# Kernel optimization log

Measured on AMD Instinct MI355X. Metric: run time of the kernel, lower is better.

Reference implementation:

```python
import jax, jax.numpy as jnp
import numpy as np
from jax import lax

EPS = 1e-5

def setup_inputs() -> dict:
    key = jax.random.key(0)
    k1, k2 = jax.random.split(key)
    x = jax.random.normal(k1, (8, 256, 64, 64), dtype=jnp.float32)
    W = jax.random.normal(k2, (128, 256, 5, 5), dtype=jnp.float32) * 0.02
    gamma = jnp.ones((128,), dtype=jnp.float32)
    beta = jnp.zeros((128,), dtype=jnp.float32)
    return {"x": x, "W": W, "gamma": gamma, "beta": beta}

def reference(x, W, gamma, beta):
    B, C, H, Wd = x.shape
    # bilinear x2 upsample, half-pixel centers (== torch align_corners=False)
    up = jax.image.resize(x, (B, C, 2 * H, 2 * Wd), method="bilinear")
    # conv2d, stride 1, padding 2, no bias (norm == 'BN')
    out = lax.conv_general_dilated(
        up, W, window_strides=(1, 1), padding=[(2, 2), (2, 2)],
        dimension_numbers=("NCHW", "OIHW", "NCHW"))
    # BatchNorm2d (batch statistics, training-style refresh)
    mean = jnp.mean(out, axis=(0, 2, 3))
    var = jnp.var(out, axis=(0, 2, 3))
    inv = gamma / jnp.sqrt(var + EPS)
    out = (out - mean[None, :, None, None]) * inv[None, :, None, None] + beta[None, :, None, None]
    # activation: torch.relu
    return jax.nn.relu(out)
```

## Files before the change

kernel.cpp:

```cpp
#include <hip/hip_runtime.h>
#include <hip/hip_bf16.h>
#include <stdint.h>

typedef short s8v __attribute__((ext_vector_type(8)));
typedef float f4v __attribute__((ext_vector_type(4)));

__device__ __align__(16) float g_zeros[4] = {0.f, 0.f, 0.f, 0.f};

__device__ __forceinline__ void async_copy16(const void* gsrc, void* lds_dst) {
  __builtin_amdgcn_global_load_lds(
      (const __attribute__((address_space(1))) uint32_t*)(uintptr_t)gsrc,
      (__attribute__((address_space(3))) uint32_t*)(uint32_t)(uintptr_t)lds_dst,
      16, 0, 0);
}

__global__ void wpack_kernel(const float* __restrict__ W, __hip_bfloat16* __restrict__ Wr) {
  int i = blockIdx.x * 256 + threadIdx.x;
  int ci = i & 255;
  int rest = i >> 8;
  int co = rest & 127;
  int pos = rest >> 7;
  Wr[i] = __float2bfloat16(W[(co * 256 + ci) * 25 + pos]);
}

__global__ __launch_bounds__(256, 2) void upsample_kernel(const float* __restrict__ x,
                                                          __hip_bfloat16* __restrict__ up) {
  __shared__ __hip_bfloat16 lx[10 * 48 * 66];
  const int tid = threadIdx.x;
  const int bx = blockIdx.x;
  const int owb = bx & 1;
  const int ohb = (bx >> 1) & 7;
  const int cb = (bx >> 4) & 3;
  const int b = bx >> 6;
  const int oh0 = ohb * 16, ow0 = owb * 64, c0 = cb * 64;
  const int ih0 = (oh0 >> 1) - 1;
  const int iw_lo = (ow0 >> 1) - 1;
  const int aligned = (iw_lo < 0 ? 0 : iw_lo) & ~15;

  for (int i = tid; i < 64 * 10 * 12; i += 256) {
    int c = i / 120;
    int rem = i - c * 120;
    int r = rem / 12;
    int w4 = (rem - r * 12) * 4;
    int gr = ih0 + r;
    gr = gr < 0 ? 0 : (gr > 63 ? 63 : gr);
    const float4 v = *(const float4*)&x[(((b * 256 + c0 + c) * 64) + gr) * 64 + aligned + w4];
    int base = (r * 48 + w4) * 66 + c;
    lx[base]       = __float2bfloat16(v.x);
    lx[base + 66]  = __float2bfloat16(v.y);
    lx[base + 132] = __float2bfloat16(v.z);
    lx[base + 198] = __float2bfloat16(v.w);
  }
  __syncthreads();

  const int c2 = (tid & 31) * 2;
  const int owq = tid >> 5;
  uint32_t* upu = (uint32_t*)up;
  for (int it = 0; it < 128; ++it) {
    int oh_l = it >> 3;
    int ow_l = (it & 7) * 8 + owq;
    int oh = oh0 + oh_l, ow = ow0 + ow_l;
    int ihA = (oh >> 1) - ((oh & 1) ^ 1);
    float wh = (oh & 1) ? 0.75f : 0.25f;
    int iwA = (ow >> 1) - ((ow & 1) ^ 1);
    float wwt = (ow & 1) ? 0.75f : 0.25f;
    int r0 = ihA - ih0;
    int w0 = (iwA < 0 ? 0 : iwA) - aligned;
    int w1t = iwA + 1; w1t = w1t > 63 ? 63 : w1t;
    int w1 = w1t - aligned;
    uint32_t t00 = *(const uint32_t*)&lx[(r0 * 48 + w0) * 66 + c2];
    uint32_t t01 = *(const uint32_t*)&lx[(r0 * 48 + w1) * 66 + c2];
    uint32_t t10 = *(const uint32_t*)&lx[((r0 + 1) * 48 + w0) * 66 + c2];
    uint32_t t11 = *(const uint32_t*)&lx[((r0 + 1) * 48 + w1) * 66 + c2];
    float wlo = wh * wwt, wlo1 = wh * (1.f - wwt);
    float whi = (1.f - wh) * wwt, whi1 = (1.f - wh) * (1.f - wwt);
    float vlo = wlo * __uint_as_float(t00 << 16) + wlo1 * __uint_as_float(t01 << 16) +
                whi * __uint_as_float(t10 << 16) + whi1 * __uint_as_float(t11 << 16);
    float vhi = wlo * __uint_as_float(t00 & 0xffff0000u) + wlo1 * __uint_as_float(t01 & 0xffff0000u) +
                whi * __uint_as_float(t10 & 0xffff0000u) + whi1 * __uint_as_float(t11 & 0xffff0000u);
    __hip_bfloat16 h0 = __float2bfloat16(vlo);
    __hip_bfloat16 h1 = __float2bfloat16(vhi);
    uint32_t pk = (uint32_t)(*(unsigned short*)&h0) | ((uint32_t)(*(unsigned short*)&h1) << 16);
    upu[((((size_t)(b * 128 + oh) * 128) + ow) * 256 + c0 + c2) >> 1] = pk;
  }
}

#define ASLOT 4608
__global__ __launch_bounds__(512, 4) void conv_kernel(const __hip_bfloat16* __restrict__ up,
                                                      const __hip_bfloat16* __restrict__ Wr,
                                                      float* __restrict__ out,
                                                      float* __restrict__ gstats) {
  __shared__ __align__(16) unsigned short lA[5 * ASLOT];
  __shared__ __align__(16) unsigned short lB[2][128 * 64];
  __shared__ float lsum[128], lssq[128];

  const int tid = threadIdx.x;
  const int lane = tid & 63;
  const int wave = tid >> 6;
  const int wm = wave >> 1;
  const int wn = wave & 1;
  const int lane15 = lane & 15;
  const int quad = lane >> 4;

  const int bid = blockIdx.x;
  const int orig = ((bid & 7) << 6) | (bid >> 3);
  const int b = orig >> 6;
  const int oh0 = ((orig >> 1) & 31) << 2;
  const int owh = orig & 1;
  const int ow0 = owh << 6;

  const f4v zero4 = {0.f, 0.f, 0.f, 0.f};
  if (tid < 128) { lsum[tid] = 0.f; lssq[tid] = 0.f; }
  if (owh == 0) {
    for (int i = tid; i < 5 * 32; i += 512) {
      int s = i >> 5, rem = i & 31;
      *(f4v*)&lA[(s * 576 + (rem >> 3) * 8 + (rem & 7)) * 8] = zero4;
    }
  } else {
    for (int i = tid; i < 5 * 48; i += 512) {
      int s = i / 48, rem = i - s * 48;
      *(f4v*)&lA[(s * 576 + (66 + (rem >> 3)) * 8 + (rem & 7)) * 8] = zero4;
    }
  }

  auto stageA = [&](int slot, const __hip_bfloat16* uprow) {
    int idx = (wave << 6) + lane;
    int r = idx >> 3, pc = idx & 7;
    int cq = pc ^ (r & 7);
    int iw = ow0 - 4 + r;
    const void* src = ((unsigned)iw < 128u) ? (const void*)(uprow + iw * 256 + cq * 8)
                                            : (const void*)g_zeros;
    async_copy16(src, (void*)&lA[(slot * 576 + (wave << 6)) * 8]);
    if (wave == 0) {
      int idx2 = 512 + lane;
      int r2 = idx2 >> 3, pc2 = idx2 & 7;
      int cq2 = pc2 ^ (r2 & 7);
      int iw2 = ow0 - 4 + r2;
      const void* src2 = ((unsigned)iw2 < 128u) ? (const void*)(uprow + iw2 * 256 + cq2 * 8)
                                                : (const void*)g_zeros;
      async_copy16(src2, (void*)&lA[(slot * 576 + 512) * 8]);
    }
  };
  auto stageB = [&](const __hip_bfloat16* wrow, int bsel) {
#pragma unroll
    for (int t = 0; t < 2; ++t) {
      int base = t * 512 + (wave << 6);
      int idx = base + lane;
      int n = idx >> 3, pc = idx & 7;
      int cq = pc ^ (n & 7);
      async_copy16(wrow + n * 256 + cq * 8, (void*)&lB[bsel][base * 8]);
    }
  };

  f4v acc[4][4];
#pragma unroll
  for (int i = 0; i < 4; ++i)
#pragma unroll
    for (int j = 0; j < 4; ++j) acc[i][j] = zero4;

  for (int rr = 0; rr < 4; ++rr) {
    int ih = oh0 + rr - 2;
    if ((unsigned)ih < 128u)
      stageA(ih % 5, up + (size_t)(b * 128 + ih) * 128 * 256);
  }
  stageB(Wr, 0);
  __syncthreads();

  int buf = 0;
  for (int cb = 0; cb < 4; ++cb) {
    const int c0 = cb << 6;
    for (int kh = 0; kh < 5; ++kh) {
      const int ih = oh0 + wm + kh - 2;
      const bool rowok = (unsigned)ih < 128u;
      const int abase = rowok ? (ih % 5) * ASLOT : 0;
      for (int kw = 0; kw < 5; ++kw) {
        const int pos = kh * 5 + kw;
        if (pos < 24) {
          stageB(Wr + (size_t)(pos + 1) * 32768 + c0, buf ^ 1);
        } else if (cb < 3) {
          stageB(Wr + (c0 + 64), buf ^ 1);
        }
        if (kw == 2 && kh < 4) {
          int ihp = oh0 + kh + 2;
          if (ihp < 128)
            stageA(ihp % 5, up + (size_t)(b * 128 + ihp) * 128 * 256 + c0);
        }
        if (rowok) {
#pragma unroll
          for (int ks = 0; ks < 2; ++ks) {
            const int cq = ks * 4 + quad;
            s8v a[4], bb[4];
#pragma unroll
            for (int mt = 0; mt < 4; ++mt) {
              int r = mt * 16 + lane15 + kw + 2;
              a[mt] = *(const s8v*)&lA[abase + (r * 8 + (cq ^ (r & 7))) * 8];
            }
#pragma unroll
            for (int nt = 0; nt < 4; ++nt) {
              int n = (wn << 6) + nt * 16 + lane15;
              bb[nt] = *(const s8v*)&lB[buf][(n * 8 + (cq ^ (n & 7))) * 8];
            }
#pragma unroll
            for (int mt = 0; mt < 4; ++mt)
#pragma unroll
              for (int nt = 0; nt < 4; ++nt)
                acc[mt][nt] = __builtin_amdgcn_mfma_f32_16x16x32_bf16(a[mt], bb[nt], acc[mt][nt], 0, 0, 0);
          }
        }
        __syncthreads();
        buf ^= 1;
      }
    }
    if (cb < 3) {
      const int c0n = (cb + 1) << 6;
      for (int rr = 0; rr < 4; ++rr) {
        int ihn = oh0 + rr - 2;
        if ((unsigned)ihn < 128u)
          stageA(ihn % 5, up + (size_t)(b * 128 + ihn) * 128 * 256 + c0n);
      }
      __syncthreads();
    }
  }

  const int oh = oh0 + wm;
#pragma unroll
  for (int nt = 0; nt < 4; ++nt) {
    const int n = (wn << 6) + nt * 16 + lane15;
    float* oc = out + ((size_t)(b * 128 + n) * 128 + oh) * 128 + ow0;
    float s = 0.f, ss = 0.f;
#pragma unroll
    for (int mt = 0; mt < 4; ++mt) {
      f4v v = acc[mt][nt];
      *(f4v*)&oc[mt * 16 + (quad << 2)] = v;
      s += v.x + v.y + v.z + v.w;
      ss += v.x * v.x + v.y * v.y + v.z * v.z + v.w * v.w;
    }
    s += __shfl_xor(s, 16, 64); ss += __shfl_xor(ss, 16, 64);
    s += __shfl_xor(s, 32, 64); ss += __shfl_xor(ss, 32, 64);
    if (quad == 0) { atomicAdd(&lsum[n], s); atomicAdd(&lssq[n], ss); }
  }
  __syncthreads();
  if (tid < 128) {
    atomicAdd(&gstats[tid], lsum[tid]);
    atomicAdd(&gstats[128 + tid], lssq[tid]);
  }
}

__global__ void scalebias_kernel(const float* __restrict__ gstats, const float* __restrict__ gamma,
                                 const float* __restrict__ beta, float* __restrict__ sb) {
  int c = threadIdx.x;
  float mean = gstats[c] * (1.f / 131072.f);
  float var = gstats[128 + c] * (1.f / 131072.f) - mean * mean;
  float inv = gamma[c] * rsqrtf(var + 1e-5f);
  sb[c] = inv;
  sb[128 + c] = beta[c] - mean * inv;
}

__global__ void norm_kernel(float* __restrict__ out, const float* __restrict__ sb) {
  int i = blockIdx.x * 256 + threadIdx.x;
  f4v v = ((f4v*)out)[i];
  int c = (i >> 12) & 127;
  float sc = sb[c], bi = sb[128 + c];
  v.x = fmaxf(fmaf(v.x, sc, bi), 0.f);
  v.y = fmaxf(fmaf(v.y, sc, bi), 0.f);
  v.z = fmaxf(fmaf(v.z, sc, bi), 0.f);
  v.w = fmaxf(fmaf(v.w, sc, bi), 0.f);
  ((f4v*)out)[i] = v;
}

extern "C" void kernel_launch(void* const* d_in, const int* in_sizes, int n_in,
                              void* d_out, int out_size, void* d_ws, size_t ws_size,
                              hipStream_t stream) {
  (void)in_sizes; (void)n_in; (void)out_size; (void)ws_size;
  const float* x = (const float*)d_in[0];
  const float* W = (const float*)d_in[1];
  const float* gamma = (const float*)d_in[2];
  const float* beta = (const float*)d_in[3];
  float* out = (float*)d_out;
  char* ws = (char*)d_ws;
  __hip_bfloat16* up = (__hip_bfloat16*)ws;
  __hip_bfloat16* Wr = (__hip_bfloat16*)(ws + 67108864);
  float* gstats = (float*)(ws + 67108864 + 1638400);
  float* sb = gstats + 256;

  hipMemsetAsync(gstats, 0, 256 * sizeof(float), stream);
  wpack_kernel<<<3200, 256, 0, stream>>>(W, Wr);
  upsample_kernel<<<512, 256, 0, stream>>>(x, up);
  conv_kernel<<<512, 512, 0, stream>>>(up, Wr, out, gstats);
  scalebias_kernel<<<1, 128, 0, stream>>>(gstats, gamma, beta, sb);
  norm_kernel<<<16384, 256, 0, stream>>>(out, sb);
}
```

Measured before the change: 339.0 us.

## Widen conv tile to full rows, use explicit vmcnt waits, fuse small kernels

The conv kernel now computes a full 128-wide output row per block (8 M-tiles per wave), which halves the block count and doubles A-tile reuse against each weight tile. The zero-padding fallback buffer is dropped in favour of zeroed halo slots in LDS. Syncthreads are replaced by explicit s_waitcnt vmcnt plus s_barrier so in-flight async loads can overlap compute, and the A restaging at channel-block boundaries moves into the main loop. Separately, the weight pack is transposed through LDS and also clears gstats, which removes the memset, and the scale/bias kernel is folded into norm. The cost is more accumulator registers and LDS per block, and occupancy drops to two blocks per CU.

```diff
diff --git a/kernel.cpp b/kernel.cpp
--- a/kernel.cpp
+++ b/kernel.cpp
@@ -4,8 +4,6 @@
 
 typedef short s8v __attribute__((ext_vector_type(8)));
 typedef float f4v __attribute__((ext_vector_type(4)));
-
-__device__ __align__(16) float g_zeros[4] = {0.f, 0.f, 0.f, 0.f};
 
 __device__ __forceinline__ void async_copy16(const void* gsrc, void* lds_dst) {
   __builtin_amdgcn_global_load_lds(
@@ -14,13 +12,29 @@
       16, 0, 0);
 }
 
-__global__ void wpack_kernel(const float* __restrict__ W, __hip_bfloat16* __restrict__ Wr) {
-  int i = blockIdx.x * 256 + threadIdx.x;
-  int ci = i & 255;
-  int rest = i >> 8;
-  int co = rest & 127;
-  int pos = rest >> 7;
-  Wr[i] = __float2bfloat16(W[(co * 256 + ci) * 25 + pos]);
+#define WAITVM(N) asm volatile("s_waitcnt vmcnt(" #N ")" ::: "memory")
+__device__ __forceinline__ void block_barrier() {
+  asm volatile("" ::: "memory");
+  __builtin_amdgcn_s_barrier();
+  asm volatile("" ::: "memory");
+}
+
+__global__ __launch_bounds__(256) void wpack_kernel(const float* __restrict__ W,
+                                                    __hip_bfloat16* __restrict__ Wr,
+                                                    float* __restrict__ gstats) {
+  __shared__ __hip_bfloat16 t[256 * 26];
+  const int co = blockIdx.x;
+  const int tid = threadIdx.x;
+  if (co == 0) gstats[tid] = 0.f;
+  const float* src = W + co * 6400;
+  for (int i = tid; i < 6400; i += 256) {
+    int ci = i / 25;
+    int pos = i - ci * 25;
+    t[ci * 26 + pos] = __float2bfloat16(src[i]);
+  }
+  __syncthreads();
+  for (int pos = 0; pos < 25; ++pos)
+    Wr[pos * 32768 + co * 256 + tid] = t[tid * 26 + pos];
 }
 
 __global__ __launch_bounds__(256, 2) void upsample_kernel(const float* __restrict__ x,
@@ -85,8 +99,8 @@
   }
 }
 
-#define ASLOT 4608
-__global__ __launch_bounds__(512, 4) void conv_kernel(const __hip_bfloat16* __restrict__ up,
+#define ASLOT 8448
+__global__ __launch_bounds__(512, 2) void conv_kernel(const __hip_bfloat16* __restrict__ up,
                                                       const __hip_bfloat16* __restrict__ Wr,
                                                       float* __restrict__ out,
                                                       float* __restrict__ gstats) {
@@ -101,67 +115,52 @@
   const int wn = wave & 1;
   const int lane15 = lane & 15;
   const int quad = lane >> 4;
+  const int wb = wave << 6;
 
   const int bid = blockIdx.x;
-  const int orig = ((bid & 7) << 6) | (bid >> 3);
-  const int b = orig >> 6;
-  const int oh0 = ((orig >> 1) & 31) << 2;
-  const int owh = orig & 1;
-  const int ow0 = owh << 6;
+  const int orig = ((bid & 7) << 5) | (bid >> 3);
+  const int b = orig >> 5;
+  const int oh0 = (orig & 31) << 2;
 
   const f4v zero4 = {0.f, 0.f, 0.f, 0.f};
   if (tid < 128) { lsum[tid] = 0.f; lssq[tid] = 0.f; }
-  if (owh == 0) {
-    for (int i = tid; i < 5 * 32; i += 512) {
-      int s = i >> 5, rem = i & 31;
-      *(f4v*)&lA[(s * 576 + (rem >> 3) * 8 + (rem & 7)) * 8] = zero4;
-    }
-  } else {
-    for (int i = tid; i < 5 * 48; i += 512) {
-      int s = i / 48, rem = i - s * 48;
-      *(f4v*)&lA[(s * 576 + (66 + (rem >> 3)) * 8 + (rem & 7)) * 8] = zero4;
-    }
+  if (tid < 160) {
+    int s = tid >> 5, j = tid & 31;
+    int rsel = j >> 3;
+    int r = (rsel < 2) ? rsel : (128 + rsel);
+    *(f4v*)&lA[s * ASLOT + (r * 8 + (j & 7)) * 8] = zero4;
   }
 
   auto stageA = [&](int slot, const __hip_bfloat16* uprow) {
-    int idx = (wave << 6) + lane;
-    int r = idx >> 3, pc = idx & 7;
-    int cq = pc ^ (r & 7);
-    int iw = ow0 - 4 + r;
-    const void* src = ((unsigned)iw < 128u) ? (const void*)(uprow + iw * 256 + cq * 8)
-                                            : (const void*)g_zeros;
-    async_copy16(src, (void*)&lA[(slot * 576 + (wave << 6)) * 8]);
-    if (wave == 0) {
-      int idx2 = 512 + lane;
-      int r2 = idx2 >> 3, pc2 = idx2 & 7;
-      int cq2 = pc2 ^ (r2 & 7);
-      int iw2 = ow0 - 4 + r2;
-      const void* src2 = ((unsigned)iw2 < 128u) ? (const void*)(uprow + iw2 * 256 + cq2 * 8)
-                                                : (const void*)g_zeros;
-      async_copy16(src2, (void*)&lA[(slot * 576 + 512) * 8]);
+#pragma unroll
+    for (int t = 0; t < 2; ++t) {
+      int pl = t * 512 + wb + lane;
+      int riw = pl >> 3, pc = pl & 7;
+      int r = riw + 2;
+      int cq = pc ^ (r & 7);
+      async_copy16(uprow + riw * 256 + cq * 8, (void*)&lA[slot * ASLOT + (16 + t * 512 + wb) * 8]);
     }
   };
-  auto stageB = [&](const __hip_bfloat16* wrow, int bsel) {
+  auto stageB = [&](const __hip_bfloat16* wsrc, int bsel) {
 #pragma unroll
     for (int t = 0; t < 2; ++t) {
-      int base = t * 512 + (wave << 6);
-      int idx = base + lane;
-      int n = idx >> 3, pc = idx & 7;
+      int pl = t * 512 + wb + lane;
+      int n = pl >> 3, pc = pl & 7;
       int cq = pc ^ (n & 7);
-      async_copy16(wrow + n * 256 + cq * 8, (void*)&lB[bsel][base * 8]);
+      async_copy16(wsrc + n * 256 + cq * 8, (void*)&lB[bsel][(t * 512 + wb) * 8]);
     }
   };
 
-  f4v acc[4][4];
-#pragma unroll
-  for (int i = 0; i < 4; ++i)
+  f4v acc[8][4];
+#pragma unroll
+  for (int i = 0; i < 8; ++i)
 #pragma unroll
     for (int j = 0; j < 4; ++j) acc[i][j] = zero4;
 
   for (int rr = 0; rr < 4; ++rr) {
     int ih = oh0 + rr - 2;
     if ((unsigned)ih < 128u)
-      stageA(ih % 5, up + (size_t)(b * 128 + ih) * 128 * 256);
+      stageA(ih % 5, up + (size_t)(b * 128 + ih) * 32768);
   }
   stageB(Wr, 0);
   __syncthreads();
@@ -175,24 +174,30 @@
       const int abase = rowok ? (ih % 5) * ASLOT : 0;
       for (int kw = 0; kw < 5; ++kw) {
         const int pos = kh * 5 + kw;
-        if (pos < 24) {
-          stageB(Wr + (size_t)(pos + 1) * 32768 + c0, buf ^ 1);
-        } else if (cb < 3) {
-          stageB(Wr + (c0 + 64), buf ^ 1);
+        if (cb != 0 && kh == 0 && kw == 0) {
+          for (int rr = 0; rr < 4; ++rr) {
+            int ihn = oh0 + rr - 2;
+            if ((unsigned)ihn < 128u)
+              stageA(ihn % 5, up + (size_t)(b * 128 + ihn) * 32768 + c0);
+          }
         }
-        if (kw == 2 && kh < 4) {
-          int ihp = oh0 + kh + 2;
-          if (ihp < 128)
-            stageA(ihp % 5, up + (size_t)(b * 128 + ihp) * 128 * 256 + c0);
-        }
+        if (pos < 24)      stageB(Wr + (size_t)(pos + 1) * 32768 + c0, buf ^ 1);
+        else if (cb < 3)   stageB(Wr + (c0 + 64), buf ^ 1);
+        const bool extraA = (kw == 2) && (kh < 4) && (oh0 + kh + 2 < 128);
+        if (extraA)
+          stageA((oh0 + kh + 2) % 5, up + (size_t)(b * 128 + oh0 + kh + 2) * 32768 + c0);
+        if (pos == 24 && cb == 3) { WAITVM(0); }
+        else if (extraA)          { WAITVM(4); }
+        else                      { WAITVM(2); }
+        block_barrier();
         if (rowok) {
 #pragma unroll
           for (int ks = 0; ks < 2; ++ks) {
             const int cq = ks * 4 + quad;
-            s8v a[4], bb[4];
-#pragma unroll
-            for (int mt = 0; mt < 4; ++mt) {
-              int r = mt * 16 + lane15 + kw + 2;
+            s8v a[8], bb[4];
+#pragma unroll
+            for (int mt = 0; mt < 8; ++mt) {
+              int r = mt * 16 + lane15 + kw;
               a[mt] = *(const s8v*)&lA[abase + (r * 8 + (cq ^ (r & 7))) * 8];
             }
 #pragma unroll
@@ -201,35 +206,27 @@
               bb[nt] = *(const s8v*)&lB[buf][(n * 8 + (cq ^ (n & 7))) * 8];
             }
 #pragma unroll
-            for (int mt = 0; mt < 4; ++mt)
+            for (int mt = 0; mt < 8; ++mt)
 #pragma unroll
               for (int nt = 0; nt < 4; ++nt)
                 acc[mt][nt] = __builtin_amdgcn_mfma_f32_16x16x32_bf16(a[mt], bb[nt], acc[mt][nt], 0, 0, 0);
           }
         }
-        __syncthreads();
+        block_barrier();
         buf ^= 1;
       }
     }
-    if (cb < 3) {
-      const int c0n = (cb + 1) << 6;
-      for (int rr = 0; rr < 4; ++rr) {
-        int ihn = oh0 + rr - 2;
-        if ((unsigned)ihn < 128u)
-          stageA(ihn % 5, up + (size_t)(b * 128 + ihn) * 128 * 256 + c0n);
-      }
-      __syncthreads();
-    }
-  }
-
+  }
+
+  __syncthreads();
   const int oh = oh0 + wm;
 #pragma unroll
   for (int nt = 0; nt < 4; ++nt) {
     const int n = (wn << 6) + nt * 16 + lane15;
-    float* oc = out + ((size_t)(b * 128 + n) * 128 + oh) * 128 + ow0;
+    float* oc = out + ((size_t)(b * 128 + n) * 128 + oh) * 128;
     float s = 0.f, ss = 0.f;
 #pragma unroll
-    for (int mt = 0; mt < 4; ++mt) {
+    for (int mt = 0; mt < 8; ++mt) {
       f4v v = acc[mt][nt];
       *(f4v*)&oc[mt * 16 + (quad << 2)] = v;
       s += v.x + v.y + v.z + v.w;
@@ -246,21 +243,21 @@
   }
 }
 
-__global__ void scalebias_kernel(const float* __restrict__ gstats, const float* __restrict__ gamma,
-                                 const float* __restrict__ beta, float* __restrict__ sb) {
-  int c = threadIdx.x;
-  float mean = gstats[c] * (1.f / 131072.f);
-  float var = gstats[128 + c] * (1.f / 131072.f) - mean * mean;
-  float inv = gamma[c] * rsqrtf(var + 1e-5f);
-  sb[c] = inv;
-  sb[128 + c] = beta[c] - mean * inv;
-}
-
-__global__ void norm_kernel(float* __restrict__ out, const float* __restrict__ sb) {
+__global__ void norm_kernel(float* __restrict__ out, const float* __restrict__ gstats,
+                            const float* __restrict__ gamma, const float* __restrict__ beta) {
+  __shared__ float ssb[2];
+  const int c = (blockIdx.x >> 4) & 127;
+  if (threadIdx.x == 0) {
+    float mean = gstats[c] * (1.f / 131072.f);
+    float var = gstats[128 + c] * (1.f / 131072.f) - mean * mean;
+    float inv = gamma[c] * rsqrtf(var + 1e-5f);
+    ssb[0] = inv;
+    ssb[1] = beta[c] - mean * inv;
+  }
+  __syncthreads();
   int i = blockIdx.x * 256 + threadIdx.x;
   f4v v = ((f4v*)out)[i];
-  int c = (i >> 12) & 127;
-  float sc = sb[c], bi = sb[128 + c];
+  float sc = ssb[0], bi = ssb[1];
   v.x = fmaxf(fmaf(v.x, sc, bi), 0.f);
   v.y = fmaxf(fmaf(v.y, sc, bi), 0.f);
   v.z = fmaxf(fmaf(v.z, sc, bi), 0.f);
@@ -281,12 +278,9 @@
   __hip_bfloat16* up = (__hip_bfloat16*)ws;
   __hip_bfloat16* Wr = (__hip_bfloat16*)(ws + 67108864);
   float* gstats = (float*)(ws + 67108864 + 1638400);
-  float* sb = gstats + 256;
-
-  hipMemsetAsync(gstats, 0, 256 * sizeof(float), stream);
-  wpack_kernel<<<3200, 256, 0, stream>>>(W, Wr);
+
+  wpack_kernel<<<128, 256, 0, stream>>>(W, Wr, gstats);
   upsample_kernel<<<512, 256, 0, stream>>>(x, up);
-  conv_kernel<<<512, 512, 0, stream>>>(up, Wr, out, gstats);
-  scalebias_kernel<<<1, 128, 0, stream>>>(gstats, gamma, beta, sb);
-  norm_kernel<<<16384, 256, 0, stream>>>(out, sb);
-}
+  conv_kernel<<<256, 512, 0, stream>>>(up, Wr, out, gstats);
+  norm_kernel<<<16384, 256, 0, stream>>>(out, gstats, gamma, beta);
+}
```

New measurement: 306.9 us. 1.1x faster.
